# Kernel optimization log

Hardware: AMD Instinct MI355X
Metric: run time of the kernel (lower is better)

The kernel has to match this reference:

```python
import jax, jax.numpy as jnp
import numpy as np

N, E, F, H, C = 50000, 800000, 128, 64, 40
EPS = 1e-12


def _l2norm(x):
    n = jnp.sqrt(jnp.sum(x * x, axis=-1, keepdims=True))
    return x / jnp.maximum(n, EPS)


def _sage_conv(x, edge_index, Wl, bl, Wr, num_nodes):
    # PyG SAGEConv, aggr='mean', normalize=True:
    #   out = lin_l(mean_{j in N(i)} x_j) + lin_r(x_i); out = l2_normalize(out)
    src, dst = edge_index[0], edge_index[1]
    msg = x[src]  # [E, F] gathered neighbor features
    agg = jax.ops.segment_sum(msg, dst, num_segments=num_nodes)
    cnt = jax.ops.segment_sum(jnp.ones((edge_index.shape[1],), x.dtype), dst,
                              num_segments=num_nodes)
    mean = agg / jnp.maximum(cnt, 1.0)[:, None]  # zero-in-degree nodes -> 0
    out = mean @ Wl + bl + x @ Wr
    return _l2norm(out)


def setup_inputs() -> dict:
    key = jax.random.key(0)
    ks = jax.random.split(key, 10)
    s = lambda fan_in: 1.0 / np.sqrt(fan_in)
    x = jax.random.normal(ks[0], (N, F), dtype=jnp.float32)
    edge_index = jax.random.randint(ks[1], (2, E), 0, N, dtype=jnp.int64)
    # conv1: SAGEConv(F -> H); lin_l has bias, lin_r has no bias
    Wl1 = jax.random.uniform(ks[2], (F, H), jnp.float32, -s(F), s(F))
    bl1 = jnp.zeros((H,), jnp.float32)
    Wr1 = jax.random.uniform(ks[3], (F, H), jnp.float32, -s(F), s(F))
    # lin1: Linear(F + H -> H)
    Wlin = jax.random.uniform(ks[4], (F + H, H), jnp.float32, -s(F + H), s(F + H))
    blin = jax.random.uniform(ks[5], (H,), jnp.float32, -s(F + H), s(F + H))
    # conv2: SAGEConv(H -> C)
    Wl2 = jax.random.uniform(ks[6], (H, C), jnp.float32, -s(H), s(H))
    bl2 = jnp.zeros((C,), jnp.float32)
    Wr2 = jax.random.uniform(ks[7], (H, C), jnp.float32, -s(H), s(H))
    return {"x": x, "edge_index": edge_index,
            "Wl1": Wl1, "bl1": bl1, "Wr1": Wr1,
            "Wlin": Wlin, "blin": blin,
            "Wl2": Wl2, "bl2": bl2, "Wr2": Wr2}


def reference(x, edge_index, Wl1, bl1, Wr1, Wlin, blin, Wl2, bl2, Wr2):
    hidden = jax.nn.relu(_sage_conv(x, edge_index, Wl1, bl1, Wr1, N))
    h = jax.nn.relu(jnp.concatenate([x, hidden], axis=1) @ Wlin + blin)
    # dropout is identity in eval mode
    out = _sage_conv(h, edge_index, Wl2, bl2, Wr2, N)
    return out
```

## Files before the change

### kernel.cpp

```cpp
#include <hip/hip_runtime.h>

static constexpr int NN = 50000;
static constexpr int NE = 800000;
static constexpr int F  = 128;
static constexpr int H  = 64;
static constexpr int C  = 40;

static constexpr int NB_BK = 8;
static constexpr int NCH   = 32;
static constexpr int ECH   = NE / NCH;
static constexpr int NBK   = NN / NB_BK;
static constexpr int NCSR  = NB_BK * NCH;
static constexpr int NT64  = (NN + 63) / 64;

typedef __attribute__((ext_vector_type(8))) short bf16x8;
typedef __attribute__((ext_vector_type(4))) float f32x4;

__device__ inline unsigned short f2bf(float f) {
  unsigned int u = __builtin_bit_cast(unsigned int, f);
  u = (u + 0x7fff + ((u >> 16) & 1)) >> 16;
  return (unsigned short)u;
}
__device__ inline float bf2f(unsigned short u) {
  return __builtin_bit_cast(float, (unsigned int)u << 16);
}


__device__ void hist_body(int bid, const int* __restrict__ ei,
                          int* __restrict__ hist, int* __restrict__ counter) {
  __shared__ int cnt[NBK];
  int i = bid & 7;
  int j = bid >> 3;
  for (int t = threadIdx.x; t < NBK; t += 256) cnt[t] = 0;
  __syncthreads();
  if (bid == 0 && threadIdx.x == 0) *counter = 0;
  int lo = i * NBK;
  const int* dst = ei + NE + j * ECH;
  for (int base = threadIdx.x * 4; base < ECH; base += 256 * 4) {
    int4 d4 = *reinterpret_cast<const int4*>(dst + base);
    if ((unsigned)(d4.x - lo) < (unsigned)NBK) atomicAdd(&cnt[d4.x - lo], 1);
    if ((unsigned)(d4.y - lo) < (unsigned)NBK) atomicAdd(&cnt[d4.y - lo], 1);
    if ((unsigned)(d4.z - lo) < (unsigned)NBK) atomicAdd(&cnt[d4.z - lo], 1);
    if ((unsigned)(d4.w - lo) < (unsigned)NBK) atomicAdd(&cnt[d4.w - lo], 1);
  }
  __syncthreads();
  int* hrow = hist + (size_t)j * NN + lo;
  for (int t = threadIdx.x; t < NBK; t += 256) hrow[t] = cnt[t];
}

__device__ void cvt_body(int bid, const float* __restrict__ x,
                         unsigned short* __restrict__ xb) {
  int id = bid * 256 + threadIdx.x;
  int ns = NT64 * 256;
  for (int i = id; i < NN * F / 4; i += ns) {
    float4 v = reinterpret_cast<const float4*>(x)[i];
    ushort4 o = {f2bf(v.x), f2bf(v.y), f2bf(v.z), f2bf(v.w)};
    reinterpret_cast<ushort4*>(xb)[i] = o;
  }
}

__device__ void scan_body(int bid, int* __restrict__ hist,
                          int* __restrict__ deg, int* __restrict__ start,
                          int* __restrict__ counter) {
  int lane = threadIdx.x & 63;
  int wid  = (bid * 256 + threadIdx.x) >> 6;
  int nchunks = (NN + 63) >> 6;
  if (wid >= nchunks) return;
  int n = (wid << 6) + lane;
  int d = 0;
  if (n < NN) {
    int run = 0;
#pragma unroll
    for (int j = 0; j < NCH; ++j) {
      int v = hist[(size_t)j * NN + n];
      hist[(size_t)j * NN + n] = run;
      run += v;
    }
    d = run;
  }
  int inc = d;
#pragma unroll
  for (int off = 1; off < 64; off <<= 1) {
    int t = __shfl_up(inc, off, 64);
    if (lane >= off) inc += t;
  }
  int total = __shfl(inc, 63, 64);
  int base = 0;
  if (lane == 63) base = atomicAdd(counter, total);
  base = __shfl(base, 63, 64);
  if (n < NN) {
    deg[n]   = d;
    start[n] = base + inc - d;
  }
}

__device__ inline void packW(const float* __restrict__ W, int J, int NT,
                             unsigned short* __restrict__ Wf, int idx) {
  int j  = idx & 7;
  int l  = (idx >> 3) & 63;
  int nt = (idx >> 9) % NT;
  int s  = idx / (512 * NT);
  int k  = s * 32 + (l >> 4) * 8 + j;
  int n  = nt * 16 + (l & 15);
  float v = (n < J) ? W[k * J + n] : 0.f;
  Wf[idx] = f2bf(v);
}

__device__ void prep_body(int bid,
                          const float* __restrict__ Wl1, const float* __restrict__ Wr1,
                          const float* __restrict__ Wlin,
                          const float* __restrict__ Wl2, const float* __restrict__ Wr2,
                          unsigned short* __restrict__ Wf1l, unsigned short* __restrict__ Wf1r,
                          unsigned short* __restrict__ Wflin,
                          unsigned short* __restrict__ Wf2l, unsigned short* __restrict__ Wf2r) {
  int id0 = bid * 256 + threadIdx.x;
  int ns  = 48 * 256;
  for (int i = id0; i < 4 * 4 * 512; i += ns) packW(Wl1, 64, 4, Wf1l, i);
  for (int i = id0; i < 4 * 4 * 512; i += ns) packW(Wr1, 64, 4, Wf1r, i);
  for (int i = id0; i < 6 * 4 * 512; i += ns) packW(Wlin, 64, 4, Wflin, i);
  for (int i = id0; i < 2 * 3 * 512; i += ns) packW(Wl2, 40, 3, Wf2l, i);
  for (int i = id0; i < 2 * 3 * 512; i += ns) packW(Wr2, 40, 3, Wf2r, i);
}

__device__ void fill2_body(int bid, const int* __restrict__ ei,
                           const int* __restrict__ hist,
                           const int* __restrict__ start,
                           int* __restrict__ csr_src) {
  __shared__ int fill[NBK];
  int i = bid & 7;
  int j = bid >> 3;
  int lo = i * NBK;
  const int* hrow = hist + (size_t)j * NN + lo;
  for (int t = threadIdx.x; t < NBK; t += 256) fill[t] = start[lo + t] + hrow[t];
  __syncthreads();
  const int* srcp = ei + j * ECH;
  const int* dstp = ei + NE + j * ECH;
  for (int base = threadIdx.x * 4; base < ECH; base += 256 * 4) {
    int4 s4 = *reinterpret_cast<const int4*>(srcp + base);
    int4 d4 = *reinterpret_cast<const int4*>(dstp + base);
    if ((unsigned)(d4.x - lo) < (unsigned)NBK) { int p = atomicAdd(&fill[d4.x - lo], 1); csr_src[p] = s4.x; }
    if ((unsigned)(d4.y - lo) < (unsigned)NBK) { int p = atomicAdd(&fill[d4.y - lo], 1); csr_src[p] = s4.y; }
    if ((unsigned)(d4.z - lo) < (unsigned)NBK) { int p = atomicAdd(&fill[d4.z - lo], 1); csr_src[p] = s4.z; }
    if ((unsigned)(d4.w - lo) < (unsigned)NBK) { int p = atomicAdd(&fill[d4.w - lo], 1); csr_src[p] = s4.w; }
  }
}


template <int K1, int K2, int JOUT, int NT, int NMAT, bool BIAS, bool RELU, bool OUTBF>
__device__ void mf_body(int bid,
                        const unsigned short* __restrict__ A1,
                        const unsigned short* __restrict__ A2,
                        const unsigned short* __restrict__ Wf0,
                        const unsigned short* __restrict__ Wf1,
                        const float* __restrict__ bias,
                        void* __restrict__ Y0v, void* __restrict__ Y1v) {
  constexpr int K   = K1 + K2;
  constexpr int NKS = K / 32;
  int lane = threadIdx.x & 63;
  int w    = __builtin_amdgcn_readfirstlane(threadIdx.x >> 6);
  int m    = lane & 15;
  int kg   = lane >> 4;
  int n0   = bid * 64;
  int row  = n0 + w * 16 + m;
  int rowc = row < NN ? row : NN - 1;

  f32x4 acc[NMAT][NT];
#pragma unroll
  for (int mt = 0; mt < NMAT; ++mt)
#pragma unroll
    for (int nt = 0; nt < NT; ++nt) acc[mt][nt] = {0.f, 0.f, 0.f, 0.f};

#pragma unroll
  for (int s = 0; s < NKS; ++s) {
    const unsigned short* Ab; int rs, koff;
    if (s * 32 < K1) { Ab = A1; rs = K1; koff = s * 32; }
    else             { Ab = A2; rs = K2; koff = s * 32 - K1; }
    bf16x8 a = *reinterpret_cast<const bf16x8*>(Ab + (size_t)rowc * rs + koff + kg * 8);
#pragma unroll
    for (int mt = 0; mt < NMAT; ++mt) {
      const unsigned short* Wf = (NMAT == 2 && mt) ? Wf1 : Wf0;
#pragma unroll
      for (int nt = 0; nt < NT; ++nt) {
        bf16x8 b = *reinterpret_cast<const bf16x8*>(Wf + (size_t)((s * NT + nt) * 64 + lane) * 8);
        acc[mt][nt] = __builtin_amdgcn_mfma_f32_16x16x32_bf16(a, b, acc[mt][nt], 0, 0, 0);
      }
    }
  }

#pragma unroll
  for (int mt = 0; mt < NMAT; ++mt) {
    void* Yv = (NMAT == 2 && mt) ? Y1v : Y0v;
#pragma unroll
    for (int nt = 0; nt < NT; ++nt) {
      int gc = nt * 16 + m;
      bool cv = gc < JOUT;
      float bb = (BIAS && cv) ? bias[gc] : 0.f;
#pragma unroll
      for (int r = 0; r < 4; ++r) {
        int grow = n0 + w * 16 + kg * 4 + r;
        if (grow < NN && cv) {
          float v = acc[mt][nt][r] + bb;
          if (RELU) v = fmaxf(v, 0.f);
          if (OUTBF) ((unsigned short*)Yv)[(size_t)grow * JOUT + gc] = f2bf(v);
          else       ((float*)Yv)[(size_t)grow * JOUT + gc] = v;
        }
      }
    }
  }
}


__global__ __launch_bounds__(256) void k_p1(const int* __restrict__ ei,
                                            int* __restrict__ hist,
                                            int* __restrict__ counter,
                                            const float* __restrict__ x,
                                            unsigned short* __restrict__ xb) {
  if (blockIdx.x < NCSR) hist_body(blockIdx.x, ei, hist, counter);
  else                   cvt_body(blockIdx.x - NCSR, x, xb);
}

__global__ __launch_bounds__(256) void k_p2(int* __restrict__ hist,
                                            int* __restrict__ deg,
                                            int* __restrict__ start,
                                            int* __restrict__ counter,
                                            const float* Wl1, const float* Wr1,
                                            const float* Wlin,
                                            const float* Wl2, const float* Wr2,
                                            unsigned short* Wf1l, unsigned short* Wf1r,
                                            unsigned short* Wflin,
                                            unsigned short* Wf2l, unsigned short* Wf2r) {
  if (blockIdx.x < 196) scan_body(blockIdx.x, hist, deg, start, counter);
  else prep_body(blockIdx.x - 196, Wl1, Wr1, Wlin, Wl2, Wr2,
                 Wf1l, Wf1r, Wflin, Wf2l, Wf2r);
}

__global__ __launch_bounds__(256) void k_p3(const int* __restrict__ ei,
                                            const int* __restrict__ hist,
                                            const int* __restrict__ start,
                                            int* __restrict__ csr_src,
                                            const unsigned short* __restrict__ xb,
                                            const unsigned short* __restrict__ Wf1l,
                                            const unsigned short* __restrict__ Wf1r,
                                            unsigned short* __restrict__ p1b,
                                            unsigned short* __restrict__ q1b) {
  if (blockIdx.x < NCSR) fill2_body(blockIdx.x, ei, hist, start, csr_src);
  else mf_body<F, 0, H, 4, 2, false, false, true>(blockIdx.x - NCSR, xb, nullptr,
                                                  Wf1l, Wf1r, nullptr, p1b, q1b);
}

template <int K1, int K2, int JOUT, int NT, int NMAT, bool BIAS, bool RELU, bool OUTBF>
__global__ __launch_bounds__(256) void k_mf(const unsigned short* __restrict__ A1,
                                            const unsigned short* __restrict__ A2,
                                            const unsigned short* __restrict__ Wf0,
                                            const unsigned short* __restrict__ Wf1,
                                            const float* __restrict__ bias,
                                            void* __restrict__ Y0v,
                                            void* __restrict__ Y1v) {
  mf_body<K1, K2, JOUT, NT, NMAT, BIAS, RELU, OUTBF>(blockIdx.x, A1, A2, Wf0, Wf1,
                                                     bias, Y0v, Y1v);
}


template <int JC, bool RELU, bool OUTBF>
__global__ __launch_bounds__(256) void k_agg(const unsigned short* __restrict__ p,
                                             const unsigned short* __restrict__ q,
                                             const float* __restrict__ bl,
                                             const int* __restrict__ deg,
                                             const int* __restrict__ start,
                                             const int* __restrict__ csr_src,
                                             void* __restrict__ outp) {
  int lane = threadIdx.x & 63;
  int wid  = (blockIdx.x * blockDim.x + threadIdx.x) >> 6;
  int nw   = (gridDim.x * blockDim.x) >> 6;
  bool jl = lane < JC;
  int lidx = jl ? lane : 0;
  for (int node = wid; node < NN; node += nw) {
    int d  = __builtin_amdgcn_readfirstlane(deg[node]);
    int st = __builtin_amdgcn_readfirstlane(start[node]);
    float acc8[8];
#pragma unroll
    for (int i = 0; i < 8; ++i) acc8[i] = 0.f;
    int t = 0;
    for (; t + 16 <= d; t += 16) {
      int s[16];
#pragma unroll
      for (int i = 0; i < 16; ++i)
        s[i] = __builtin_amdgcn_readfirstlane(csr_src[st + t + i]);
      unsigned short v[16];
#pragma unroll
      for (int i = 0; i < 16; ++i) v[i] = p[(size_t)s[i] * JC + lidx];
#pragma unroll
      for (int i = 0; i < 16; ++i) acc8[i & 7] += bf2f(v[i]);
    }
    for (; t + 4 <= d; t += 4) {
      int s0 = __builtin_amdgcn_readfirstlane(csr_src[st + t + 0]);
      int s1 = __builtin_amdgcn_readfirstlane(csr_src[st + t + 1]);
      int s2 = __builtin_amdgcn_readfirstlane(csr_src[st + t + 2]);
      int s3 = __builtin_amdgcn_readfirstlane(csr_src[st + t + 3]);
      unsigned short v0 = p[(size_t)s0 * JC + lidx];
      unsigned short v1 = p[(size_t)s1 * JC + lidx];
      unsigned short v2 = p[(size_t)s2 * JC + lidx];
      unsigned short v3 = p[(size_t)s3 * JC + lidx];
      acc8[0] += bf2f(v0); acc8[1] += bf2f(v1);
      acc8[2] += bf2f(v2); acc8[3] += bf2f(v3);
    }
    for (; t < d; ++t) {
      int s = __builtin_amdgcn_readfirstlane(csr_src[st + t]);
      acc8[0] += bf2f(p[(size_t)s * JC + lidx]);
    }
    float acc = ((acc8[0] + acc8[1]) + (acc8[2] + acc8[3])) +
                ((acc8[4] + acc8[5]) + (acc8[6] + acc8[7]));
    float mean = acc / fmaxf((float)d, 1.0f);
    float v = 0.f;
    if (jl) v = mean + bl[lidx] + bf2f(q[(size_t)node * JC + lidx]);
    float ss = v * v;
#pragma unroll
    for (int off = 32; off > 0; off >>= 1) ss += __shfl_xor(ss, off, 64);
    v = v / fmaxf(sqrtf(ss), 1e-12f);
    if (RELU) v = fmaxf(v, 0.f);
    if (jl) {
      if (OUTBF) ((unsigned short*)outp)[(size_t)node * JC + lidx] = f2bf(v);
      else       ((float*)outp)[(size_t)node * JC + lidx] = v;
    }
  }
}


static inline size_t align256(size_t x) { return (x + 255) & ~(size_t)255; }

extern "C" void kernel_launch(void* const* d_in, const int* in_sizes, int n_in,
                              void* d_out, int out_size, void* d_ws, size_t ws_size,
                              hipStream_t stream) {
  const float* x    = (const float*)d_in[0];
  const int*   ei   = (const int*)d_in[1];
  const float* Wl1  = (const float*)d_in[2];
  const float* bl1  = (const float*)d_in[3];
  const float* Wr1  = (const float*)d_in[4];
  const float* Wlin = (const float*)d_in[5];
  const float* blin = (const float*)d_in[6];
  const float* Wl2  = (const float*)d_in[7];
  const float* bl2  = (const float*)d_in[8];
  const float* Wr2  = (const float*)d_in[9];
  float* out = (float*)d_out;

  char* w = (char*)d_ws;
  size_t off = 0;
  int* deg     = (int*)(w + off); off += align256((size_t)NN * 4);
  int* start   = (int*)(w + off); off += align256((size_t)NN * 4);
  int* counter = (int*)(w + off); off += 256;
  int* csr_src = (int*)(w + off); off += align256((size_t)NE * 4);
  int* hist    = (int*)(w + off); off += align256((size_t)NCH * NN * 4);
  unsigned short* xb      = (unsigned short*)(w + off); off += align256((size_t)NN * F * 2);
  unsigned short* hiddenb = (unsigned short*)(w + off); off += align256((size_t)NN * H * 2);
  unsigned short* hb      = (unsigned short*)(w + off); off += align256((size_t)NN * H * 2);
  unsigned short* p1b = (unsigned short*)(w + off); off += align256((size_t)NN * H * 2);
  unsigned short* q1b = (unsigned short*)(w + off); off += align256((size_t)NN * H * 2);
  unsigned short* p2b = (unsigned short*)(w + off); off += align256((size_t)NN * C * 2);
  unsigned short* q2b = (unsigned short*)(w + off); off += align256((size_t)NN * C * 2);
  unsigned short* Wf1l  = (unsigned short*)(w + off); off += align256(4 * 4 * 512 * 2);
  unsigned short* Wf1r  = (unsigned short*)(w + off); off += align256(4 * 4 * 512 * 2);
  unsigned short* Wflin = (unsigned short*)(w + off); off += align256(6 * 4 * 512 * 2);
  unsigned short* Wf2l  = (unsigned short*)(w + off); off += align256(2 * 3 * 512 * 2);
  unsigned short* Wf2r  = (unsigned short*)(w + off); off += align256(2 * 3 * 512 * 2);

  const int T = 256;

  k_p1<<<NCSR + NT64, T, 0, stream>>>(ei, hist, counter, x, xb);
  k_p2<<<244, T, 0, stream>>>(hist, deg, start, counter,
                              Wl1, Wr1, Wlin, Wl2, Wr2,
                              Wf1l, Wf1r, Wflin, Wf2l, Wf2r);
  k_p3<<<NCSR + NT64, T, 0, stream>>>(ei, hist, start, csr_src,
                                      xb, Wf1l, Wf1r, p1b, q1b);
  k_agg<H, true, true><<<2048, T, 0, stream>>>(p1b, q1b, bl1, deg, start, csr_src, hiddenb);
  k_mf<F, H, H, 4, 1, true, true, true><<<NT64, T, 0, stream>>>(
      xb, hiddenb, Wflin, nullptr, blin, hb, nullptr);
  k_mf<H, 0, C, 3, 2, false, false, true><<<NT64, T, 0, stream>>>(
      hb, nullptr, Wf2l, Wf2r, nullptr, p2b, q2b);
  k_agg<C, false, false><<<2048, T, 0, stream>>>(p2b, q2b, bl2, deg, start, csr_src, out);
}
```

Baseline: 209.3 us.

## Vectorize neighbor aggregation with 8-wide bf16 loads and pad layer-2 features to 64

Rewrites the aggregation kernel so each wavefront handles 8 edges at once: lanes are split into 8 edges by 8 column chunks, each lane loads 16 bytes of bf16 features, and partial sums are combined across edges with shuffles. Previously one scalar 2-byte load was issued per lane per edge. To allow the fixed 64-element row stride, the layer-2 p/q buffers and packed weights are padded from 40 to 64 columns, and the second projection GEMM now writes 64 columns. This reduces the number of gather instructions and the scalar index reads, at the cost of extra bytes for the padded layer-2 rows and more shuffle reductions.

```diff
diff --git a/kernel.cpp b/kernel.cpp
--- a/kernel.cpp
+++ b/kernel.cpp
@@ -14,6 +14,7 @@
 static constexpr int NT64  = (NN + 63) / 64;
 
 typedef __attribute__((ext_vector_type(8))) short bf16x8;
+typedef __attribute__((ext_vector_type(8))) unsigned short u16x8;
 typedef __attribute__((ext_vector_type(4))) float f32x4;
 
 __device__ inline unsigned short f2bf(float f) {
@@ -118,8 +119,8 @@
   for (int i = id0; i < 4 * 4 * 512; i += ns) packW(Wl1, 64, 4, Wf1l, i);
   for (int i = id0; i < 4 * 4 * 512; i += ns) packW(Wr1, 64, 4, Wf1r, i);
   for (int i = id0; i < 6 * 4 * 512; i += ns) packW(Wlin, 64, 4, Wflin, i);
-  for (int i = id0; i < 2 * 3 * 512; i += ns) packW(Wl2, 40, 3, Wf2l, i);
-  for (int i = id0; i < 2 * 3 * 512; i += ns) packW(Wr2, 40, 3, Wf2r, i);
+  for (int i = id0; i < 2 * 4 * 512; i += ns) packW(Wl2, 40, 4, Wf2l, i);
+  for (int i = id0; i < 2 * 4 * 512; i += ns) packW(Wr2, 40, 4, Wf2r, i);
 }
 
 __device__ void fill2_body(int bid, const int* __restrict__ ei,
@@ -261,66 +262,104 @@
 }
 
 
-template <int JC, bool RELU, bool OUTBF>
-__global__ __launch_bounds__(256) void k_agg(const unsigned short* __restrict__ p,
-                                             const unsigned short* __restrict__ q,
-                                             const float* __restrict__ bl,
-                                             const int* __restrict__ deg,
-                                             const int* __restrict__ start,
-                                             const int* __restrict__ csr_src,
-                                             void* __restrict__ outp) {
+template <int JCR, bool RELU, bool OUTBF>
+__global__ __launch_bounds__(256) void k_aggv(const unsigned short* __restrict__ p,
+                                              const unsigned short* __restrict__ q,
+                                              const float* __restrict__ bl,
+                                              const int* __restrict__ deg,
+                                              const int* __restrict__ start,
+                                              const int* __restrict__ csr_src,
+                                              void* __restrict__ outp) {
+  constexpr int ST = 64;
   int lane = threadIdx.x & 63;
-  int wid  = (blockIdx.x * blockDim.x + threadIdx.x) >> 6;
-  int nw   = (gridDim.x * blockDim.x) >> 6;
-  bool jl = lane < JC;
-  int lidx = jl ? lane : 0;
+  int e = lane >> 3, c = lane & 7;
+  int wid = (blockIdx.x * blockDim.x + threadIdx.x) >> 6;
+  int nw  = (gridDim.x * blockDim.x) >> 6;
+
+  float blv[8];
+#pragma unroll
+  for (int j = 0; j < 8; ++j) {
+    int f = c * 8 + j;
+    blv[j] = (f < JCR) ? bl[f] : 0.f;
+  }
+
   for (int node = wid; node < NN; node += nw) {
     int d  = __builtin_amdgcn_readfirstlane(deg[node]);
     int st = __builtin_amdgcn_readfirstlane(start[node]);
-    float acc8[8];
-#pragma unroll
-    for (int i = 0; i < 8; ++i) acc8[i] = 0.f;
-    int t = 0;
-    for (; t + 16 <= d; t += 16) {
-      int s[16];
-#pragma unroll
-      for (int i = 0; i < 16; ++i)
-        s[i] = __builtin_amdgcn_readfirstlane(csr_src[st + t + i]);
-      unsigned short v[16];
-#pragma unroll
-      for (int i = 0; i < 16; ++i) v[i] = p[(size_t)s[i] * JC + lidx];
-#pragma unroll
-      for (int i = 0; i < 16; ++i) acc8[i & 7] += bf2f(v[i]);
-    }
-    for (; t + 4 <= d; t += 4) {
-      int s0 = __builtin_amdgcn_readfirstlane(csr_src[st + t + 0]);
-      int s1 = __builtin_amdgcn_readfirstlane(csr_src[st + t + 1]);
-      int s2 = __builtin_amdgcn_readfirstlane(csr_src[st + t + 2]);
-      int s3 = __builtin_amdgcn_readfirstlane(csr_src[st + t + 3]);
-      unsigned short v0 = p[(size_t)s0 * JC + lidx];
-      unsigned short v1 = p[(size_t)s1 * JC + lidx];
-      unsigned short v2 = p[(size_t)s2 * JC + lidx];
-      unsigned short v3 = p[(size_t)s3 * JC + lidx];
-      acc8[0] += bf2f(v0); acc8[1] += bf2f(v1);
-      acc8[2] += bf2f(v2); acc8[3] += bf2f(v3);
-    }
-    for (; t < d; ++t) {
-      int s = __builtin_amdgcn_readfirstlane(csr_src[st + t]);
-      acc8[0] += bf2f(p[(size_t)s * JC + lidx]);
-    }
-    float acc = ((acc8[0] + acc8[1]) + (acc8[2] + acc8[3])) +
-                ((acc8[4] + acc8[5]) + (acc8[6] + acc8[7]));
-    float mean = acc / fmaxf((float)d, 1.0f);
-    float v = 0.f;
-    if (jl) v = mean + bl[lidx] + bf2f(q[(size_t)node * JC + lidx]);
-    float ss = v * v;
-#pragma unroll
-    for (int off = 32; off > 0; off >>= 1) ss += __shfl_xor(ss, off, 64);
-    v = v / fmaxf(sqrtf(ss), 1e-12f);
-    if (RELU) v = fmaxf(v, 0.f);
-    if (jl) {
-      if (OUTBF) ((unsigned short*)outp)[(size_t)node * JC + lidx] = f2bf(v);
-      else       ((float*)outp)[(size_t)node * JC + lidx] = v;
+    float a0[8], a1[8];
+#pragma unroll
+    for (int j = 0; j < 8; ++j) { a0[j] = 0.f; a1[j] = 0.f; }
+    int r = 0;
+    for (; r + 16 <= d; r += 16) {
+      int i0 = csr_src[st + r + e];
+      int i1 = csr_src[st + r + 8 + e];
+      u16x8 v0 = *reinterpret_cast<const u16x8*>(p + (size_t)i0 * ST + c * 8);
+      u16x8 v1 = *reinterpret_cast<const u16x8*>(p + (size_t)i1 * ST + c * 8);
+#pragma unroll
+      for (int j = 0; j < 8; ++j) { a0[j] += bf2f(v0[j]); a1[j] += bf2f(v1[j]); }
+    }
+    if (r + 8 <= d) {
+      int i0 = csr_src[st + r + e];
+      u16x8 v0 = *reinterpret_cast<const u16x8*>(p + (size_t)i0 * ST + c * 8);
+#pragma unroll
+      for (int j = 0; j < 8; ++j) a0[j] += bf2f(v0[j]);
+      r += 8;
+    }
+    int rem = d - r;
+    if (rem > 0) {
+      int ec = e < rem ? e : rem - 1;
+      int i0 = csr_src[st + r + ec];
+      u16x8 v0 = *reinterpret_cast<const u16x8*>(p + (size_t)i0 * ST + c * 8);
+      if (e < rem) {
+#pragma unroll
+        for (int j = 0; j < 8; ++j) a0[j] += bf2f(v0[j]);
+      }
+    }
+#pragma unroll
+    for (int j = 0; j < 8; ++j) a0[j] += a1[j];
+#pragma unroll
+    for (int ms = 8; ms <= 32; ms <<= 1)
+#pragma unroll
+      for (int j = 0; j < 8; ++j) a0[j] += __shfl_xor(a0[j], ms, 64);
+
+    float inv = 1.f / fmaxf((float)d, 1.f);
+    u16x8 qv = *reinterpret_cast<const u16x8*>(q + (size_t)node * ST + c * 8);
+    float v[8];
+    float ss = 0.f;
+#pragma unroll
+    for (int j = 0; j < 8; ++j) {
+      int f = c * 8 + j;
+      float t = a0[j] * inv + blv[j] + bf2f(qv[j]);
+      if (f >= JCR) t = 0.f;
+      v[j] = t;
+      ss += t * t;
+    }
+#pragma unroll
+    for (int ms = 1; ms <= 4; ms <<= 1) ss += __shfl_xor(ss, ms, 64);
+    float rn = 1.f / fmaxf(sqrtf(ss), 1e-12f);
+
+    if (e == 0 && c * 8 < JCR) {
+      if (OUTBF) {
+        u16x8 o;
+#pragma unroll
+        for (int j = 0; j < 8; ++j) {
+          float t = v[j] * rn;
+          if (RELU) t = fmaxf(t, 0.f);
+          o[j] = f2bf(t);
+        }
+        *reinterpret_cast<u16x8*>((unsigned short*)outp + (size_t)node * JCR + c * 8) = o;
+      } else {
+        float* op = (float*)outp + (size_t)node * JCR + c * 8;
+#pragma unroll
+        for (int j = 0; j < 8; j += 4) {
+          float4 o = {v[j] * rn, v[j + 1] * rn, v[j + 2] * rn, v[j + 3] * rn};
+          if (RELU) {
+            o.x = fmaxf(o.x, 0.f); o.y = fmaxf(o.y, 0.f);
+            o.z = fmaxf(o.z, 0.f); o.w = fmaxf(o.w, 0.f);
+          }
+          *reinterpret_cast<float4*>(op + j) = o;
+        }
+      }
     }
   }
 }
@@ -353,15 +392,15 @@
   unsigned short* xb      = (unsigned short*)(w + off); off += align256((size_t)NN * F * 2);
   unsigned short* hiddenb = (unsigned short*)(w + off); off += align256((size_t)NN * H * 2);
   unsigned short* hb      = (unsigned short*)(w + off); off += align256((size_t)NN * H * 2);
-  unsigned short* p1b = (unsigned short*)(w + off); off += align256((size_t)NN * H * 2);
-  unsigned short* q1b = (unsigned short*)(w + off); off += align256((size_t)NN * H * 2);
-  unsigned short* p2b = (unsigned short*)(w + off); off += align256((size_t)NN * C * 2);
-  unsigned short* q2b = (unsigned short*)(w + off); off += align256((size_t)NN * C * 2);
+  unsigned short* p1b = (unsigned short*)(w + off); off += align256((size_t)NN * 64 * 2);
+  unsigned short* q1b = (unsigned short*)(w + off); off += align256((size_t)NN * 64 * 2);
+  unsigned short* p2b = (unsigned short*)(w + off); off += align256((size_t)NN * 64 * 2);
+  unsigned short* q2b = (unsigned short*)(w + off); off += align256((size_t)NN * 64 * 2);
   unsigned short* Wf1l  = (unsigned short*)(w + off); off += align256(4 * 4 * 512 * 2);
   unsigned short* Wf1r  = (unsigned short*)(w + off); off += align256(4 * 4 * 512 * 2);
   unsigned short* Wflin = (unsigned short*)(w + off); off += align256(6 * 4 * 512 * 2);
-  unsigned short* Wf2l  = (unsigned short*)(w + off); off += align256(2 * 3 * 512 * 2);
-  unsigned short* Wf2r  = (unsigned short*)(w + off); off += align256(2 * 3 * 512 * 2);
+  unsigned short* Wf2l  = (unsigned short*)(w + off); off += align256(2 * 4 * 512 * 2);
+  unsigned short* Wf2r  = (unsigned short*)(w + off); off += align256(2 * 4 * 512 * 2);
 
   const int T = 256;
 
@@ -371,10 +410,10 @@
                               Wf1l, Wf1r, Wflin, Wf2l, Wf2r);
   k_p3<<<NCSR + NT64, T, 0, stream>>>(ei, hist, start, csr_src,
                                       xb, Wf1l, Wf1r, p1b, q1b);
-  k_agg<H, true, true><<<2048, T, 0, stream>>>(p1b, q1b, bl1, deg, start, csr_src, hiddenb);
+  k_aggv<H, true, true><<<2048, T, 0, stream>>>(p1b, q1b, bl1, deg, start, csr_src, hiddenb);
   k_mf<F, H, H, 4, 1, true, true, true><<<NT64, T, 0, stream>>>(
       xb, hiddenb, Wflin, nullptr, blin, hb, nullptr);
-  k_mf<H, 0, C, 3, 2, false, false, true><<<NT64, T, 0, stream>>>(
+  k_mf<H, 0, 64, 4, 2, false, false, true><<<NT64, T, 0, stream>>>(
       hb, nullptr, Wf2l, Wf2r, nullptr, p2b, q2b);
-  k_agg<C, false, false><<<2048, T, 0, stream>>>(p2b, q2b, bl2, deg, start, csr_src, out);
-}
+  k_aggv<C, false, false><<<2048, T, 0, stream>>>(p2b, q2b, bl2, deg, start, csr_src, out);
+}
```

Result: faster. 205.1 us, median of 3 (-2.0%).
